# Kernel optimization log

Hardware: AMD Instinct MI355X
Metric: run time of the kernel (lower is better)

## Reference

```python
import jax, jax.numpy as jnp
import numpy as np
from jax import lax

DIM, HEADS, POOL = 512, 8, 16
HD = DIM // HEADS
SCALE = HD ** -0.5


def _cbs(x, w, s, b, d=1, g=1):
    """Conv2d(bias=False, pad=d*(k-1)//2) + folded BN (scale,bias) + SiLU."""
    k = w.shape[-1]
    p = d * (k - 1) // 2
    y = lax.conv_general_dilated(x, w, (1, 1), [(p, p), (p, p)],
                                 rhs_dilation=(d, d), feature_group_count=g,
                                 dimension_numbers=("NCHW", "OIHW", "NCHW"))
    y = y * s[None, :, None, None] + b[None, :, None, None]
    return y * jax.nn.sigmoid(y)  # SiLU


def _forward(x, w01, s01, b01, w02, s02, b02, w03, s03, b03,
             w12, s12, b12, w13, s13, b13, w22, s22, b22, w23, s23, b23,
             w3, s3, b3, wkv, skv, bkv, wfc1, bfc1, wfc2, bfc2):
    bsz, c, h, w = x.shape
    # ---- _MutilScal ----
    a01 = _cbs(x, w01, s01, b01)                       # [b,128,h,w]
    a03 = _cbs(_cbs(a01, w02, s02, b02, d=3, g=128), w03, s03, b03)
    a13 = _cbs(_cbs(a01, w12, s12, b12, d=5, g=128), w13, s13, b13)
    a23 = _cbs(_cbs(a01, w22, s22, b22, d=7, g=128), w23, s23, b23)
    attn = _cbs(a03 + a13 + a23, w3, s3, b3) * x       # [b,512,h,w]
    # AdaptiveAvgPool2d(POOL): exact block mean since h,w divisible by POOL
    pooled = attn.reshape(bsz, c, POOL, h // POOL, POOL, w // POOL).mean(axis=(3, 5))
    kv = _cbs(pooled, wkv, skv, bkv)                   # [b,1024,16,16]
    # ---- pooled cross-attention ----
    n, n1 = h * w, POOL * POOL
    q = x.reshape(bsz, HEADS, HD, n).transpose(0, 1, 3, 2)          # [b,H,n,d]
    kvr = kv.reshape(bsz, 2, HEADS, HD, n1)
    k = kvr[:, 0].transpose(0, 1, 3, 2)                              # [b,H,n1,d]
    v = kvr[:, 1].transpose(0, 1, 3, 2)                              # [b,H,n1,d]
    dots = jnp.einsum("bhnd,bhmd->bhnm", q, k) * SCALE
    a = jax.nn.softmax(dots, axis=-1)
    o = jnp.einsum("bhnm,bhmd->bhnd", a, v)                          # [b,H,n,d]
    attn_out = o.transpose(0, 1, 3, 2).reshape(bsz, c, h, w)
    # ---- SE channel gate ----
    gap = x.mean(axis=(2, 3))                                        # [b,c]
    y = jnp.clip(gap @ wfc1[:, :, 0, 0].T + bfc1, 0.0, 6.0)          # ReLU6
    gate = jax.nn.sigmoid(y @ wfc2[:, :, 0, 0].T + bfc2)             # [b,c]
    c_attn = gate[:, :, None, None] * x
    return attn_out + c_attn


def setup_inputs() -> dict:
    key = jax.random.key(0)
    ks = jax.random.split(key, 32)
    ki = iter(ks)
    f = jnp.float32

    def rn(shape, scale=0.05):
        return (jax.random.normal(next(ki), shape, dtype=f) * scale)

    inp = {"x": jax.random.normal(next(ki), (8, DIM, 64, 64), dtype=f)}
    inp.update(w01=rn((128, 512, 1, 1)), s01=jnp.ones((128,), f), b01=rn((128,)))
    inp.update(w02=rn((128, 1, 3, 3)), s02=jnp.ones((128,), f), b02=rn((128,)))
    inp.update(w03=rn((512, 128, 1, 1)), s03=jnp.ones((512,), f), b03=rn((512,)))
    inp.update(w12=rn((128, 1, 3, 3)), s12=jnp.ones((128,), f), b12=rn((128,)))
    inp.update(w13=rn((512, 128, 1, 1)), s13=jnp.ones((512,), f), b13=rn((512,)))
    inp.update(w22=rn((128, 1, 3, 3)), s22=jnp.ones((128,), f), b22=rn((128,)))
    inp.update(w23=rn((512, 128, 1, 1)), s23=jnp.ones((512,), f), b23=rn((512,)))
    inp.update(w3=rn((512, 512, 1, 1)), s3=jnp.ones((512,), f), b3=rn((512,)))
    inp.update(wkv=rn((1024, 512, 1, 1)), skv=jnp.ones((1024,), f), bkv=rn((1024,)))
    inp.update(wfc1=rn((128, 512, 1, 1)), bfc1=rn((128,)))
    inp.update(wfc2=rn((512, 128, 1, 1)), bfc2=rn((512,)))
    return inp


def reference(x, w01, s01, b01, w02, s02, b02, w03, s03, b03,
              w12, s12, b12, w13, s13, b13, w22, s22, b22, w23, s23, b23,
              w3, s3, b3, wkv, skv, bkv, wfc1, bfc1, wfc2, bfc2):
    return _forward(x, w01, s01, b01, w02, s02, b02, w03, s03, b03,
                    w12, s12, b12, w13, s13, b13, w22, s22, b22, w23, s23, b23,
                    w3, s3, b3, wkv, skv, bkv, wfc1, bfc1, wfc2, bfc2)
```

## Files before the change

kernel.cpp:

```cpp
#include <hip/hip_runtime.h>
#include <cstddef>


static __device__ __forceinline__ float silu_f(float v) {
  return v / (1.f + __expf(-v));
}

typedef __attribute__((ext_vector_type(8))) short short8v;
typedef __attribute__((ext_vector_type(4))) float f32x4;

union FragU { unsigned u[4]; short8v v; uint4 q; };

static __device__ __forceinline__ unsigned short f2bf(float f) {
  unsigned u = __builtin_bit_cast(unsigned, f);
  u += 0x7fffu + ((u >> 16) & 1u);
  return (unsigned short)(u >> 16);
}
static __device__ __forceinline__ unsigned packbf(float lo, float hi) {
  return (unsigned)f2bf(lo) | ((unsigned)f2bf(hi) << 16);
}
static __device__ __forceinline__ float bf_lo(unsigned w) {
  return __builtin_bit_cast(float, w << 16);
}
static __device__ __forceinline__ float bf_hi(unsigned w) {
  return __builtin_bit_cast(float, w & 0xffff0000u);
}

static __device__ __forceinline__ void gload16(const unsigned* gsrc, unsigned* ldst) {
  __builtin_amdgcn_global_load_lds(
      (const __attribute__((address_space(1))) unsigned*)gsrc,
      (__attribute__((address_space(3))) unsigned*)ldst, 16, 0, 0);
}

static __device__ __forceinline__ void stage_tile_g(const unsigned* __restrict__ src,
                                                    unsigned* dst, int tid) {
  gload16(src + 4 * tid, dst + 4 * tid);
  gload16(src + 4 * (tid + 512), dst + 4 * (tid + 512));
}

static __device__ __forceinline__ short8v load_frag4(const unsigned* P, int ksg, int pos) {
  FragU f;
  f.q = *(const uint4*)(P + (((ksg << 7) + pos) << 2));
  return f.v;
}

static __device__ __forceinline__ void stage_x_pack(const float* __restrict__ src, int ld,
                                                    unsigned* Xp, int tid) {
  const int pos = tid & 127, kg = tid >> 7;
  const float* p = src + pos + (size_t)(kg * 16) * ld;
  float v[16];
#pragma unroll
  for (int i = 0; i < 16; ++i) v[i] = p[(size_t)i * ld];
#pragma unroll
  for (int i2 = 0; i2 < 4; ++i2) {
    const int kq = kg * 4 + i2;
    const int r4 = (kq & 3) + ((kq >> 3) << 2);
    const int sub = (kq >> 2) & 1;
    uint2 wv;
    wv.x = packbf(v[i2 * 4 + 0], v[i2 * 4 + 1]);
    wv.y = packbf(v[i2 * 4 + 2], v[i2 * 4 + 3]);
    *(uint2*)(Xp + (((r4 << 7) + pos) << 2) + sub * 2) = wv;
  }
}

#define GEMM_IDS                                            \
  const int tid = threadIdx.x;                              \
  const int w = tid >> 6, lane = tid & 63;                  \
  const int g = lane >> 4, nl = lane & 15;                  \
  const int wr = w >> 1, wc = w & 1;

#define GEMM_KSTEP(ACC)                                                            \
  _Pragma("unroll")                                                                \
  for (int ks = 0; ks < 2; ++ks) {                                                 \
    const short8v a0 = load_frag4(Wp, ks * 4 + g, wr * 32 + nl);                   \
    const short8v a1 = load_frag4(Wp, ks * 4 + g, wr * 32 + 16 + nl);              \
    _Pragma("unroll")                                                              \
    for (int jj = 0; jj < 4; ++jj) {                                               \
      const short8v bfr = load_frag4(Xp, ks * 4 + g, wc * 64 + jj * 16 + nl);      \
      ACC[0][jj] = __builtin_amdgcn_mfma_f32_16x16x32_bf16(a0, bfr, ACC[0][jj], 0, 0, 0); \
      ACC[1][jj] = __builtin_amdgcn_mfma_f32_16x16x32_bf16(a1, bfr, ACC[1][jj], 0, 0, 0); \
    }                                                                              \
  }

__global__ __launch_bounds__(256)
void prepack_w_kernel(const float* __restrict__ w01, const float* __restrict__ w03,
                      const float* __restrict__ w13, const float* __restrict__ w23,
                      const float* __restrict__ w3, const float* __restrict__ wkv,
                      unsigned* __restrict__ img)
{
  const int t = blockIdx.x;
  const float* W; int K; int tile; unsigned* base;
  if (t < 8)       { W = w01; K = 512; tile = t;      base = img; }
  else if (t < 16) { W = w03; K = 128; tile = t - 8;  base = img + 32768; }
  else if (t < 24) { W = w13; K = 128; tile = t - 16; base = img + 65536; }
  else if (t < 32) { W = w23; K = 128; tile = t - 24; base = img + 98304; }
  else if (t < 64) { W = w3;  K = 512; tile = t - 32; base = img + 131072; }
  else             { W = wkv; K = 512; tile = t - 64; base = img + 262144; }
  const int nk = K >> 6;
  const int to = tile / nk, tk = tile - to * nk;
  unsigned* dst = base + (size_t)tile * 4096;
  for (int wi = threadIdx.x; wi < 4096; wi += 256) {
    const int r4 = wi >> 9, pos = (wi >> 2) & 127, sub = (wi >> 1) & 1, j = wi & 1;
    const int kq = (r4 & 3) + sub * 4 + ((r4 >> 2) << 3);
    const int k = tk * 64 + 4 * kq + 2 * j;
    const int oc = to * 128 + pos;
    dst[wi] = packbf(W[(size_t)oc * K + k], W[(size_t)oc * K + k + 1]);
  }
}

__global__ __launch_bounds__(512)
void gemm_a01_kernel(const float* __restrict__ X, const unsigned* __restrict__ Wimg,
                     const float* __restrict__ sc, const float* __restrict__ bi,
                     unsigned* __restrict__ A01p)
{
  const int b = blockIdx.z, p0 = blockIdx.x * 128;
  GEMM_IDS
  __shared__ unsigned Xp[4096], Wp[4096];

  f32x4 acc[2][4];
#pragma unroll
  for (int i = 0; i < 2; ++i)
#pragma unroll
    for (int jj = 0; jj < 4; ++jj) acc[i][jj] = (f32x4){0.f, 0.f, 0.f, 0.f};

  for (int ks8 = 0; ks8 < 8; ++ks8) {
    __syncthreads();
    stage_x_pack(X + (size_t)b * 512 * 4096 + (size_t)(ks8 * 64) * 4096 + p0, 4096, Xp, tid);
    stage_tile_g(Wimg + (size_t)ks8 * 4096, Wp, tid);
    __syncthreads();
    GEMM_KSTEP(acc)
  }

#pragma unroll
  for (int i = 0; i < 2; ++i) {
    const int base = wr * 32 + i * 16 + 4 * g;
    const float s0_ = sc[base + 0], b0_ = bi[base + 0];
    const float s1_ = sc[base + 1], b1_ = bi[base + 1];
    const float s2_ = sc[base + 2], b2_ = bi[base + 2];
    const float s3_ = sc[base + 3], b3_ = bi[base + 3];
#pragma unroll
    for (int jj = 0; jj < 4; ++jj) {
      const int pos = p0 + wc * 64 + jj * 16 + nl;
      const float v0 = silu_f(s0_ * acc[i][jj][0] + b0_);
      const float v1 = silu_f(s1_ * acc[i][jj][1] + b1_);
      const float v2 = silu_f(s2_ * acc[i][jj][2] + b2_);
      const float v3 = silu_f(s3_ * acc[i][jj][3] + b3_);
      A01p[((size_t)b * 64 + (base >> 1)) * 4096 + pos]     = packbf(v0, v1);
      A01p[((size_t)b * 64 + (base >> 1) + 1) * 4096 + pos] = packbf(v2, v3);
    }
  }
}

__global__ __launch_bounds__(256)
void dwconv_pack_kernel(const unsigned* __restrict__ A01p, unsigned* __restrict__ Timg,
                        const float* __restrict__ w02, const float* __restrict__ s02, const float* __restrict__ b02,
                        const float* __restrict__ w12, const float* __restrict__ s12, const float* __restrict__ b12,
                        const float* __restrict__ w22, const float* __restrict__ s22, const float* __restrict__ b22)
{
  const int br = blockIdx.z;
  const int yb = blockIdx.y;
  const int b = yb >> 4, t16 = yb & 15, kstep = t16 >> 3, mm = t16 & 7;
  const int kq = (mm & 3) + ((mm >> 2) << 3);
  const int cbase = kstep * 64 + kq * 4;
  const int p = blockIdx.x * 256 + threadIdx.x;
  const int y = p >> 6, xx = p & 63;
  const int d = 3 + 2 * br;

  const float* wsel = br == 0 ? w02 : (br == 1 ? w12 : w22);
  const float* ssel = br == 0 ? s02 : (br == 1 ? s12 : s22);
  const float* bsel = br == 0 ? b02 : (br == 1 ? b12 : b22);

  float sum[8] = {};
  const unsigned* plane0 = A01p + ((size_t)b * 64 + (cbase >> 1)) * 4096;

#pragma unroll
  for (int u = -1; u <= 1; ++u) {
    const int yv = y + u * d;
    if ((unsigned)yv < 64u) {
#pragma unroll
      for (int v = -1; v <= 1; ++v) {
        const int xv = xx + v * d;
        if ((unsigned)xv < 64u) {
          const int idx = yv * 64 + xv;
          const int tap = (u + 1) * 3 + (v + 1);
#pragma unroll
          for (int q = 0; q < 4; ++q) {
            const int sub = q >> 1, jw = q & 1;
            const unsigned wv = plane0[(size_t)(sub * 8 + jw) * 4096 + idx];
            const int ch = cbase + sub * 16 + jw * 2;
            sum[q * 2 + 0] += wsel[(ch + 0) * 9 + tap] * bf_lo(wv);
            sum[q * 2 + 1] += wsel[(ch + 1) * 9 + tap] * bf_hi(wv);
          }
        }
      }
    }
  }

  unsigned wout[4];
#pragma unroll
  for (int h = 0; h < 4; ++h) {
    const int ch = cbase + (h >> 1) * 16 + (h & 1) * 2;
    const float va = silu_f(ssel[ch] * sum[h * 2] + bsel[ch]);
    const float vb = silu_f(ssel[ch + 1] * sum[h * 2 + 1] + bsel[ch + 1]);
    wout[h] = packbf(va, vb);
  }
  const int tile = ((br * 8 + b) * 2 + kstep) * 32 + (p >> 7);
  *(uint4*)(Timg + (size_t)tile * 4096 + (((mm << 7) + (p & 127)) << 2)) = *(uint4*)wout;
}

__global__ __launch_bounds__(512)
void gemm3branch_img_kernel(const unsigned* __restrict__ Timg, const unsigned* __restrict__ Wimg3,
                            const float* __restrict__ s0, const float* __restrict__ s1, const float* __restrict__ s2,
                            const float* __restrict__ b0, const float* __restrict__ b1, const float* __restrict__ b2,
                            unsigned* __restrict__ Bimg)
{
  const int b = blockIdx.z, pt = blockIdx.x, oc0 = blockIdx.y * 128;
  GEMM_IDS
  __shared__ unsigned Xp[4096], Wp[4096];

  float sum[2][4][4] = {};

#pragma unroll
  for (int brn = 0; brn < 3; ++brn) {
    const float* ss = brn == 0 ? s0 : (brn == 1 ? s1 : s2);
    const float* bs = brn == 0 ? b0 : (brn == 1 ? b1 : b2);

    f32x4 acc[2][4];
#pragma unroll
    for (int i = 0; i < 2; ++i)
#pragma unroll
      for (int jj = 0; jj < 4; ++jj) acc[i][jj] = (f32x4){0.f, 0.f, 0.f, 0.f};

#pragma unroll
    for (int ksx = 0; ksx < 2; ++ksx) {
      __syncthreads();
      stage_tile_g(Timg + (((size_t)(brn * 8 + b) * 2 + ksx) * 32 + pt) * 4096, Xp, tid);
      stage_tile_g(Wimg3 + (size_t)brn * 32768 + ((size_t)(oc0 >> 7) * 2 + ksx) * 4096, Wp, tid);
      __syncthreads();
      GEMM_KSTEP(acc)
    }

#pragma unroll
    for (int i = 0; i < 2; ++i) {
      const int base = oc0 + wr * 32 + i * 16 + 4 * g;
#pragma unroll
      for (int r = 0; r < 4; ++r) {
        const float s = ss[base + r], bb = bs[base + r];
#pragma unroll
        for (int jj = 0; jj < 4; ++jj)
          sum[i][jj][r] += silu_f(s * acc[i][jj][r] + bb);
      }
    }
  }

#pragma unroll
  for (int i = 0; i < 2; ++i) {
    const int ol = wr * 32 + i * 16 + 4 * g;
    const int kstep_g = (oc0 + ol) >> 6;
    const int kin = ol & 63;
    const int kq2 = kin >> 2;
    const int r4 = (kq2 & 3) + ((kq2 >> 3) << 2);
    const int sub = (kq2 >> 2) & 1;
#pragma unroll
    for (int jj = 0; jj < 4; ++jj) {
      const int pos = wc * 64 + jj * 16 + nl;
      uint2 wv;
      wv.x = packbf(sum[i][jj][0], sum[i][jj][1]);
      wv.y = packbf(sum[i][jj][2], sum[i][jj][3]);
      *(uint2*)(Bimg + ((size_t)(b * 8 + kstep_g) * 32 + pt) * 4096 + (((r4 << 7) + pos) << 2) + sub * 2) = wv;
    }
  }
}

__global__ __launch_bounds__(512)
void gemm_pool_img_kernel(const unsigned* __restrict__ Bimg, const unsigned* __restrict__ W3img,
                          const float* __restrict__ sc, const float* __restrict__ bi,
                          const float* __restrict__ xin, float* __restrict__ pooled)
{
  const int b = blockIdx.z, pt = blockIdx.x, oc0 = blockIdx.y * 128;
  const int p0 = pt * 128;
  const float* xb = xin + (size_t)b * 512 * 4096;
  GEMM_IDS
  __shared__ unsigned Xp[4096], Wp[4096];

  f32x4 acc[2][4];
#pragma unroll
  for (int i = 0; i < 2; ++i)
#pragma unroll
    for (int jj = 0; jj < 4; ++jj) acc[i][jj] = (f32x4){0.f, 0.f, 0.f, 0.f};

  for (int ks8 = 0; ks8 < 8; ++ks8) {
    __syncthreads();
    stage_tile_g(Bimg + ((size_t)(b * 8 + ks8) * 32 + pt) * 4096, Xp, tid);
    stage_tile_g(W3img + ((size_t)(oc0 >> 7) * 8 + ks8) * 4096, Wp, tid);
    __syncthreads();
    GEMM_KSTEP(acc)
  }

#pragma unroll
  for (int i = 0; i < 2; ++i)
#pragma unroll
    for (int r = 0; r < 4; ++r) {
      const int oc = oc0 + wr * 32 + i * 16 + 4 * g + r;
      const float s = sc[oc], bb = bi[oc];
#pragma unroll
      for (int jj = 0; jj < 4; ++jj) {
        const int p = p0 + wc * 64 + jj * 16 + nl;
        float val = silu_f(s * acc[i][jj][r] + bb) * xb[(size_t)oc * 4096 + p];
        val += __shfl_xor(val, 1, 64);
        val += __shfl_xor(val, 2, 64);
        if ((nl & 3) == 0) {
          const int y = p >> 6, col = p & 63;
          atomicAdd(&pooled[((size_t)b * 512 + oc) * 256 + (y >> 2) * 16 + (col >> 2)],
                    val * (1.f / 16.f));
        }
      }
    }
}

__global__ __launch_bounds__(512)
void gemm_kv_kernel(const float* __restrict__ X, const unsigned* __restrict__ WKVimg,
                    const float* __restrict__ sc, const float* __restrict__ bi,
                    unsigned* __restrict__ Kimg, unsigned* __restrict__ Vimg)
{
  const int b = blockIdx.z, p0 = blockIdx.x * 128, oc0 = blockIdx.y * 128;
  const float* Xb = X + (size_t)b * 512 * 256;
  GEMM_IDS
  __shared__ unsigned Xp[4096], Wp[4096];

  f32x4 acc[2][4];
#pragma unroll
  for (int i = 0; i < 2; ++i)
#pragma unroll
    for (int jj = 0; jj < 4; ++jj) acc[i][jj] = (f32x4){0.f, 0.f, 0.f, 0.f};

  for (int ks8 = 0; ks8 < 8; ++ks8) {
    __syncthreads();
    stage_x_pack(Xb + (size_t)(ks8 * 64) * 256 + p0, 256, Xp, tid);
    stage_tile_g(WKVimg + ((size_t)(oc0 >> 7) * 8 + ks8) * 4096, Wp, tid);
    __syncthreads();
    GEMM_KSTEP(acc)
  }

  const bool isK = (oc0 < 512);
#pragma unroll
  for (int i = 0; i < 2; ++i) {
    const int ocb = oc0 + wr * 32 + i * 16 + 4 * g;
#pragma unroll
    for (int jj = 0; jj < 4; ++jj) {
      const int pos = p0 + wc * 64 + jj * 16 + nl;
      float v[4];
#pragma unroll
      for (int r = 0; r < 4; ++r)
        v[r] = silu_f(sc[ocb + r] * acc[i][jj][r] + bi[ocb + r]);
      const int ch = pos >> 7, ml = pos & 127;
      if (isK) {
        const int h = ocb >> 6, d0 = ocb & 63;
        const int kq = d0 >> 2, sub = (kq >> 2) & 1;
        const int r4 = (kq & 3) + ((kq >> 3) << 2);
        unsigned* t = Kimg + ((size_t)(b * 8 + h) * 2 + ch) * 4096;
        uint2 wv;
        wv.x = packbf(v[0] * 0.125f, v[1] * 0.125f);
        wv.y = packbf(v[2] * 0.125f, v[3] * 0.125f);
        *(uint2*)(t + (((r4 << 7) + ml) << 2) + sub * 2) = wv;
      } else {
        const int h = (ocb - 512) >> 6, d0 = (ocb - 512) & 63;
        unsigned* t = Vimg + ((size_t)(b * 8 + h) * 2 + ch) * 4096;
        float ov[4];
#pragma unroll
        for (int r = 0; r < 4; ++r) ov[r] = __shfl_xor(v[r], 1, 64);
        if ((nl & 1) == 0) {
          const int s = (ml >> 1) & 1, m4 = ml >> 2;
#pragma unroll
          for (int r = 0; r < 4; ++r)
            t[((m4 * 64 + d0 + r) << 1) + s] = packbf(v[r], ov[r]);
        }
      }
    }
  }
}

__global__ __launch_bounds__(256)
void gap_kernel(const float* __restrict__ x, float* __restrict__ gap)
{
  const int bc = blockIdx.x;
  const int tid = threadIdx.x;
  const float* p = x + (size_t)bc * 4096;
  float v = 0.f;
#pragma unroll
  for (int j = 0; j < 16; ++j) v += p[j * 256 + tid];
#pragma unroll
  for (int off = 32; off >= 1; off >>= 1) v += __shfl_down(v, off, 64);
  __shared__ float red[4];
  if ((tid & 63) == 0) red[tid >> 6] = v;
  __syncthreads();
  if (tid == 0) gap[bc] = (red[0] + red[1] + red[2] + red[3]) * (1.f / 4096.f);
}

__global__ __launch_bounds__(512)
void se_kernel(const float* __restrict__ gap,
               const float* __restrict__ wfc1, const float* __restrict__ bfc1,
               const float* __restrict__ wfc2, const float* __restrict__ bfc2,
               float* __restrict__ gate)
{
  const int b = blockIdx.x, tid = threadIdx.x;
  __shared__ float ylds[128];
  if (tid < 128) {
    float a = 0.f;
    for (int c = 0; c < 512; ++c) a += gap[b * 512 + c] * wfc1[tid * 512 + c];
    a += bfc1[tid];
    ylds[tid] = fminf(fmaxf(a, 0.f), 6.f);
  }
  __syncthreads();
  float g = 0.f;
  for (int j = 0; j < 128; ++j) g += ylds[j] * wfc2[tid * 128 + j];
  g += bfc2[tid];
  gate[b * 512 + tid] = 1.f / (1.f + __expf(-g));
}

__global__ __launch_bounds__(512)
void attn_mfma_kernel(const float* __restrict__ x, const unsigned* __restrict__ Kimg,
                      const unsigned* __restrict__ Vimg,
                      const float* __restrict__ gate, float* __restrict__ out)
{
  const int b = blockIdx.z, h = blockIdx.y;
  const int n0 = blockIdx.x * 128;
  const int tid = threadIdx.x;
  const int w = tid >> 6, lane = tid & 63;
  const int g = lane >> 4, nl = lane & 15;

  __shared__ unsigned lds[20480];
  unsigned* Qp = lds;
  unsigned* Kb0 = lds + 4096;
  unsigned* Kb1 = lds + 8192;
  unsigned* Vb0 = lds + 12288;
  unsigned* Vb1 = lds + 16384;
  float* Osm = (float*)(lds + 4096);

  const size_t tbase = (size_t)(b * 8 + h) * 2 * 4096;

  stage_tile_g(Kimg + tbase, Kb0, tid);
  stage_tile_g(Vimg + tbase, Vb0, tid);
  stage_x_pack(x + ((size_t)b * 512 + h * 64) * 4096 + n0, 4096, Qp, tid);
  __syncthreads();
  stage_tile_g(Kimg + tbase + 4096, Kb1, tid);
  stage_tile_g(Vimg + tbase + 4096, Vb1, tid);

  float m_run = -1e30f, l_run = 0.f;
  f32x4 o[4];
#pragma unroll
  for (int i = 0; i < 4; ++i) o[i] = (f32x4){0.f, 0.f, 0.f, 0.f};

#pragma unroll
  for (int ch = 0; ch < 2; ++ch) {
    const unsigned* Kp = ch ? Kb1 : Kb0;
    const unsigned* Vp = ch ? Vb1 : Vb0;

    f32x4 s[8];
#pragma unroll
    for (int mb = 0; mb < 8; ++mb) s[mb] = (f32x4){0.f, 0.f, 0.f, 0.f};
#pragma unroll
    for (int ks = 0; ks < 2; ++ks) {
      const short8v qf = load_frag4(Qp, ks * 4 + g, w * 16 + nl);
#pragma unroll
      for (int mb = 0; mb < 8; ++mb) {
        const short8v kf = load_frag4(Kp, ks * 4 + g, mb * 16 + nl);
        s[mb] = __builtin_amdgcn_mfma_f32_16x16x32_bf16(kf, qf, s[mb], 0, 0, 0);
      }
    }

    float cm = -1e30f;
#pragma unroll
    for (int mb = 0; mb < 8; ++mb)
#pragma unroll
      for (int r = 0; r < 4; ++r) cm = fmaxf(cm, s[mb][r]);
    cm = fmaxf(cm, __shfl_xor(cm, 16, 64));
    cm = fmaxf(cm, __shfl_xor(cm, 32, 64));
    const float mnew = fmaxf(m_run, cm);
    const float corr = __expf(m_run - mnew);
    m_run = mnew;
    float cs = 0.f;
#pragma unroll
    for (int mb = 0; mb < 8; ++mb)
#pragma unroll
      for (int r = 0; r < 4; ++r) {
        const float p = __expf(s[mb][r] - mnew);
        s[mb][r] = p;
        cs += p;
      }
    cs += __shfl_xor(cs, 16, 64);
    cs += __shfl_xor(cs, 32, 64);
    l_run = l_run * corr + cs;
#pragma unroll
    for (int db = 0; db < 4; ++db)
#pragma unroll
      for (int r = 0; r < 4; ++r) o[db][r] *= corr;

#pragma unroll
    for (int ks = 0; ks < 4; ++ks) {
      FragU pf;
      pf.u[0] = packbf(s[2 * ks][0],     s[2 * ks][1]);
      pf.u[1] = packbf(s[2 * ks][2],     s[2 * ks][3]);
      pf.u[2] = packbf(s[2 * ks + 1][0], s[2 * ks + 1][1]);
      pf.u[3] = packbf(s[2 * ks + 1][2], s[2 * ks + 1][3]);
#pragma unroll
      for (int db = 0; db < 4; ++db) {
        FragU vf;
        const uint2 lo = *(const uint2*)(Vp + ((8 * ks + g) * 64 + db * 16 + nl) * 2);
        const uint2 hi = *(const uint2*)(Vp + ((8 * ks + 4 + g) * 64 + db * 16 + nl) * 2);
        vf.u[0] = lo.x; vf.u[1] = lo.y; vf.u[2] = hi.x; vf.u[3] = hi.y;
        o[db] = __builtin_amdgcn_mfma_f32_16x16x32_bf16(vf.v, pf.v, o[db], 0, 0, 0);
      }
    }
    __syncthreads();
  }

  const float inv = 1.f / l_run;
#pragma unroll
  for (int db = 0; db < 4; ++db)
#pragma unroll
    for (int r = 0; r < 4; ++r)
      Osm[(db * 16 + 4 * g + r) * 132 + w * 16 + nl] = o[db][r] * inv;
  __syncthreads();

  {
    const int n = tid & 127, t7 = tid >> 7;
    const int jw = t7 >> 1, half = t7 & 1;
#pragma unroll
    for (int i = 0; i < 16; ++i) {
      const int d = t7 + 4 * i;
      const int r4 = (i & 3) + ((i >> 3) << 2);
      const int sub = (i >> 2) & 1;
      const unsigned xw = Qp[(((r4 << 7) + n) << 2) + sub * 2 + jw];
      const float xv = half ? bf_hi(xw) : bf_lo(xw);
      const int c2 = h * 64 + d;
      const size_t off = ((size_t)b * 512 + c2) * 4096 + n0 + n;
      out[off] = Osm[d * 132 + n] + gate[b * 512 + c2] * xv;
    }
  }
}

extern "C" void kernel_launch(void* const* d_in, const int* in_sizes, int n_in,
                              void* d_out, int out_size, void* d_ws, size_t ws_size,
                              hipStream_t stream)
{
  const float* x    = (const float*)d_in[0];
  const float* w01  = (const float*)d_in[1];
  const float* s01  = (const float*)d_in[2];
  const float* b01  = (const float*)d_in[3];
  const float* w02  = (const float*)d_in[4];
  const float* s02  = (const float*)d_in[5];
  const float* b02  = (const float*)d_in[6];
  const float* w03  = (const float*)d_in[7];
  const float* s03  = (const float*)d_in[8];
  const float* b03  = (const float*)d_in[9];
  const float* w12  = (const float*)d_in[10];
  const float* s12  = (const float*)d_in[11];
  const float* b12  = (const float*)d_in[12];
  const float* w13  = (const float*)d_in[13];
  const float* s13  = (const float*)d_in[14];
  const float* b13  = (const float*)d_in[15];
  const float* w22  = (const float*)d_in[16];
  const float* s22  = (const float*)d_in[17];
  const float* b22  = (const float*)d_in[18];
  const float* w23  = (const float*)d_in[19];
  const float* s23  = (const float*)d_in[20];
  const float* b23  = (const float*)d_in[21];
  const float* w3   = (const float*)d_in[22];
  const float* s3   = (const float*)d_in[23];
  const float* b3   = (const float*)d_in[24];
  const float* wkv  = (const float*)d_in[25];
  const float* skv  = (const float*)d_in[26];
  const float* bkv  = (const float*)d_in[27];
  const float* wfc1 = (const float*)d_in[28];
  const float* bfc1 = (const float*)d_in[29];
  const float* wfc2 = (const float*)d_in[30];
  const float* bfc2 = (const float*)d_in[31];

  float* out = (float*)d_out;
  unsigned* wsu = (unsigned*)d_ws;

  unsigned* Timg   = wsu;
  float*    pooled = (float*)(wsu + 6291456);
  unsigned* Kimg   = wsu + 7340032;
  unsigned* Vimg   = wsu + 7864320;
  float*    gapb   = (float*)(wsu + 8388608);
  float*    gateb  = (float*)(wsu + 8392704);
  unsigned* Wimg   = wsu + 8396800;

  unsigned* A01p = (unsigned*)d_out;
  unsigned* Bimg = (unsigned*)d_out;

  prepack_w_kernel<<<128, 256, 0, stream>>>(w01, w03, w13, w23, w3, wkv, Wimg);
  gemm_a01_kernel<<<dim3(32, 1, 8), 512, 0, stream>>>(x, Wimg, s01, b01, A01p);
  dwconv_pack_kernel<<<dim3(16, 128, 3), 256, 0, stream>>>(A01p, Timg,
      w02, s02, b02, w12, s12, b12, w22, s22, b22);
  gemm3branch_img_kernel<<<dim3(32, 4, 8), 512, 0, stream>>>(Timg, Wimg + 32768,
      s03, s13, s23, b03, b13, b23, Bimg);
  hipMemsetAsync(pooled, 0, (size_t)1048576 * sizeof(float), stream);
  gemm_pool_img_kernel<<<dim3(32, 4, 8), 512, 0, stream>>>(Bimg, Wimg + 131072,
      s3, b3, x, pooled);
  gemm_kv_kernel<<<dim3(2, 8, 8), 512, 0, stream>>>(pooled, Wimg + 262144, skv, bkv, Kimg, Vimg);
  gap_kernel<<<4096, 256, 0, stream>>>(x, gapb);
  se_kernel<<<8, 512, 0, stream>>>(gapb, wfc1, bfc1, wfc2, bfc2, gateb);
  attn_mfma_kernel<<<dim3(32, 8, 8), 512, 0, stream>>>(x, Kimg, Vimg, gateb, out);
}
```

Baseline: 280.0 us.

## Double-buffer LDS tiles in GEMM kernels to overlap loads with MFMA

Four GEMM kernels now use two LDS buffers for the X and W tiles. Each loop step issues the next tile's global loads (async global_load_lds, plus register prefetch of the fp32 X values) before running the MFMAs on the current buffer, and keeps one barrier per step instead of two. The three-branch kernel is flattened into a single six-step pipelined loop, with the per-branch SiLU epilogue folded in. The aim is to hide global-memory latency behind compute, at the cost of twice the shared memory per block, which may lower occupancy, and more registers for the prefetched X values.

```diff
diff --git a/kernel.cpp b/kernel.cpp
--- a/kernel.cpp
+++ b/kernel.cpp
@@ -44,13 +44,15 @@
   return f.v;
 }
 
-static __device__ __forceinline__ void stage_x_pack(const float* __restrict__ src, int ld,
-                                                    unsigned* Xp, int tid) {
+static __device__ __forceinline__ void xload16(const float* __restrict__ src, int ld,
+                                               int tid, float v[16]) {
   const int pos = tid & 127, kg = tid >> 7;
   const float* p = src + pos + (size_t)(kg * 16) * ld;
-  float v[16];
 #pragma unroll
   for (int i = 0; i < 16; ++i) v[i] = p[(size_t)i * ld];
+}
+static __device__ __forceinline__ void xwrite16(const float v[16], unsigned* Xp, int tid) {
+  const int pos = tid & 127, kg = tid >> 7;
 #pragma unroll
   for (int i2 = 0; i2 < 4; ++i2) {
     const int kq = kg * 4 + i2;
@@ -63,20 +65,27 @@
   }
 }
 
+static __device__ __forceinline__ void stage_x_pack(const float* __restrict__ src, int ld,
+                                                    unsigned* Xp, int tid) {
+  float v[16];
+  xload16(src, ld, tid, v);
+  xwrite16(v, Xp, tid);
+}
+
 #define GEMM_IDS                                            \
   const int tid = threadIdx.x;                              \
   const int w = tid >> 6, lane = tid & 63;                  \
   const int g = lane >> 4, nl = lane & 15;                  \
   const int wr = w >> 1, wc = w & 1;
 
-#define GEMM_KSTEP(ACC)                                                            \
+#define GEMM_KSTEP_B(ACC, XB, WB)                                                  \
   _Pragma("unroll")                                                                \
   for (int ks = 0; ks < 2; ++ks) {                                                 \
-    const short8v a0 = load_frag4(Wp, ks * 4 + g, wr * 32 + nl);                   \
-    const short8v a1 = load_frag4(Wp, ks * 4 + g, wr * 32 + 16 + nl);              \
+    const short8v a0 = load_frag4(WB, ks * 4 + g, wr * 32 + nl);                   \
+    const short8v a1 = load_frag4(WB, ks * 4 + g, wr * 32 + 16 + nl);              \
     _Pragma("unroll")                                                              \
     for (int jj = 0; jj < 4; ++jj) {                                               \
-      const short8v bfr = load_frag4(Xp, ks * 4 + g, wc * 64 + jj * 16 + nl);      \
+      const short8v bfr = load_frag4(XB, ks * 4 + g, wc * 64 + jj * 16 + nl);      \
       ACC[0][jj] = __builtin_amdgcn_mfma_f32_16x16x32_bf16(a0, bfr, ACC[0][jj], 0, 0, 0); \
       ACC[1][jj] = __builtin_amdgcn_mfma_f32_16x16x32_bf16(a1, bfr, ACC[1][jj], 0, 0, 0); \
     }                                                                              \
@@ -115,7 +124,8 @@
 {
   const int b = blockIdx.z, p0 = blockIdx.x * 128;
   GEMM_IDS
-  __shared__ unsigned Xp[4096], Wp[4096];
+  __shared__ unsigned Xp[2][4096], Wp[2][4096];
+  const float* Xbase = X + (size_t)b * 512 * 4096 + p0;
 
   f32x4 acc[2][4];
 #pragma unroll
@@ -123,12 +133,24 @@
 #pragma unroll
     for (int jj = 0; jj < 4; ++jj) acc[i][jj] = (f32x4){0.f, 0.f, 0.f, 0.f};
 
-  for (int ks8 = 0; ks8 < 8; ++ks8) {
+  {
+    float vx[16];
+    xload16(Xbase, 4096, tid, vx);
+    stage_tile_g(Wimg, Wp[0], tid);
+    xwrite16(vx, Xp[0], tid);
+  }
+  __syncthreads();
+
+  for (int st = 0; st < 8; ++st) {
+    const int cur = st & 1;
+    float vn[16];
+    if (st < 7) {
+      xload16(Xbase + (size_t)((st + 1) * 64) * 4096, 4096, tid, vn);
+      stage_tile_g(Wimg + (size_t)(st + 1) * 4096, Wp[cur ^ 1], tid);
+    }
+    GEMM_KSTEP_B(acc, Xp[cur], Wp[cur])
+    if (st < 7) xwrite16(vn, Xp[cur ^ 1], tid);
     __syncthreads();
-    stage_x_pack(X + (size_t)b * 512 * 4096 + (size_t)(ks8 * 64) * 4096 + p0, 4096, Xp, tid);
-    stage_tile_g(Wimg + (size_t)ks8 * 4096, Wp, tid);
-    __syncthreads();
-    GEMM_KSTEP(acc)
   }
 
 #pragma unroll
@@ -216,42 +238,51 @@
 {
   const int b = blockIdx.z, pt = blockIdx.x, oc0 = blockIdx.y * 128;
   GEMM_IDS
-  __shared__ unsigned Xp[4096], Wp[4096];
+  __shared__ unsigned Xp[2][4096], Wp[2][4096];
 
   float sum[2][4][4] = {};
-
-#pragma unroll
-  for (int brn = 0; brn < 3; ++brn) {
-    const float* ss = brn == 0 ? s0 : (brn == 1 ? s1 : s2);
-    const float* bs = brn == 0 ? b0 : (brn == 1 ? b1 : b2);
-
-    f32x4 acc[2][4];
-#pragma unroll
-    for (int i = 0; i < 2; ++i)
-#pragma unroll
-      for (int jj = 0; jj < 4; ++jj) acc[i][jj] = (f32x4){0.f, 0.f, 0.f, 0.f};
-
-#pragma unroll
-    for (int ksx = 0; ksx < 2; ++ksx) {
-      __syncthreads();
-      stage_tile_g(Timg + (((size_t)(brn * 8 + b) * 2 + ksx) * 32 + pt) * 4096, Xp, tid);
-      stage_tile_g(Wimg3 + (size_t)brn * 32768 + ((size_t)(oc0 >> 7) * 2 + ksx) * 4096, Wp, tid);
-      __syncthreads();
-      GEMM_KSTEP(acc)
-    }
-
-#pragma unroll
-    for (int i = 0; i < 2; ++i) {
-      const int base = oc0 + wr * 32 + i * 16 + 4 * g;
-#pragma unroll
-      for (int r = 0; r < 4; ++r) {
-        const float s = ss[base + r], bb = bs[base + r];
-#pragma unroll
-        for (int jj = 0; jj < 4; ++jj)
-          sum[i][jj][r] += silu_f(s * acc[i][jj][r] + bb);
+  f32x4 acc[2][4];
+#pragma unroll
+  for (int i = 0; i < 2; ++i)
+#pragma unroll
+    for (int jj = 0; jj < 4; ++jj) acc[i][jj] = (f32x4){0.f, 0.f, 0.f, 0.f};
+
+#define SRC_X3(st) (Timg + (((size_t)(((st) >> 1) * 8 + b) * 2 + ((st) & 1)) * 32 + pt) * 4096)
+#define SRC_W3(st) (Wimg3 + (size_t)((st) >> 1) * 32768 + ((size_t)(oc0 >> 7) * 2 + ((st) & 1)) * 4096)
+
+  stage_tile_g(SRC_X3(0), Xp[0], tid);
+  stage_tile_g(SRC_W3(0), Wp[0], tid);
+  __syncthreads();
+
+  for (int st = 0; st < 6; ++st) {
+    const int cur = st & 1;
+    if (st < 5) {
+      stage_tile_g(SRC_X3(st + 1), Xp[cur ^ 1], tid);
+      stage_tile_g(SRC_W3(st + 1), Wp[cur ^ 1], tid);
+    }
+    GEMM_KSTEP_B(acc, Xp[cur], Wp[cur])
+    if (st & 1) {
+      const int brn = st >> 1;
+      const float* ss = brn == 0 ? s0 : (brn == 1 ? s1 : s2);
+      const float* bs = brn == 0 ? b0 : (brn == 1 ? b1 : b2);
+#pragma unroll
+      for (int i = 0; i < 2; ++i) {
+        const int base = oc0 + wr * 32 + i * 16 + 4 * g;
+#pragma unroll
+        for (int r = 0; r < 4; ++r) {
+          const float s = ss[base + r], bb = bs[base + r];
+#pragma unroll
+          for (int jj = 0; jj < 4; ++jj) {
+            sum[i][jj][r] += silu_f(s * acc[i][jj][r] + bb);
+            acc[i][jj][r] = 0.f;
+          }
+        }
       }
     }
-  }
+    __syncthreads();
+  }
+#undef SRC_X3
+#undef SRC_W3
 
 #pragma unroll
   for (int i = 0; i < 2; ++i) {
@@ -281,7 +312,7 @@
   const int p0 = pt * 128;
   const float* xb = xin + (size_t)b * 512 * 4096;
   GEMM_IDS
-  __shared__ unsigned Xp[4096], Wp[4096];
+  __shared__ unsigned Xp[2][4096], Wp[2][4096];
 
   f32x4 acc[2][4];
 #pragma unroll
@@ -289,13 +320,24 @@
 #pragma unroll
     for (int jj = 0; jj < 4; ++jj) acc[i][jj] = (f32x4){0.f, 0.f, 0.f, 0.f};
 
-  for (int ks8 = 0; ks8 < 8; ++ks8) {
+#define SRC_XP(st) (Bimg + ((size_t)(b * 8 + (st)) * 32 + pt) * 4096)
+#define SRC_WP(st) (W3img + ((size_t)(oc0 >> 7) * 8 + (st)) * 4096)
+
+  stage_tile_g(SRC_XP(0), Xp[0], tid);
+  stage_tile_g(SRC_WP(0), Wp[0], tid);
+  __syncthreads();
+
+  for (int st = 0; st < 8; ++st) {
+    const int cur = st & 1;
+    if (st < 7) {
+      stage_tile_g(SRC_XP(st + 1), Xp[cur ^ 1], tid);
+      stage_tile_g(SRC_WP(st + 1), Wp[cur ^ 1], tid);
+    }
+    GEMM_KSTEP_B(acc, Xp[cur], Wp[cur])
     __syncthreads();
-    stage_tile_g(Bimg + ((size_t)(b * 8 + ks8) * 32 + pt) * 4096, Xp, tid);
-    stage_tile_g(W3img + ((size_t)(oc0 >> 7) * 8 + ks8) * 4096, Wp, tid);
-    __syncthreads();
-    GEMM_KSTEP(acc)
-  }
+  }
+#undef SRC_XP
+#undef SRC_WP
 
 #pragma unroll
   for (int i = 0; i < 2; ++i)
@@ -324,9 +366,9 @@
                     unsigned* __restrict__ Kimg, unsigned* __restrict__ Vimg)
 {
   const int b = blockIdx.z, p0 = blockIdx.x * 128, oc0 = blockIdx.y * 128;
-  const float* Xb = X + (size_t)b * 512 * 256;
+  const float* Xb = X + (size_t)b * 512 * 256 + p0;
   GEMM_IDS
-  __shared__ unsigned Xp[4096], Wp[4096];
+  __shared__ unsigned Xp[2][4096], Wp[2][4096];
 
   f32x4 acc[2][4];
 #pragma unroll
@@ -334,12 +376,24 @@
 #pragma unroll
     for (int jj = 0; jj < 4; ++jj) acc[i][jj] = (f32x4){0.f, 0.f, 0.f, 0.f};
 
-  for (int ks8 = 0; ks8 < 8; ++ks8) {
+  {
+    float vx[16];
+    xload16(Xb, 256, tid, vx);
+    stage_tile_g(WKVimg + (size_t)(oc0 >> 7) * 8 * 4096, Wp[0], tid);
+    xwrite16(vx, Xp[0], tid);
+  }
+  __syncthreads();
+
+  for (int st = 0; st < 8; ++st) {
+    const int cur = st & 1;
+    float vn[16];
+    if (st < 7) {
+      xload16(Xb + (size_t)((st + 1) * 64) * 256, 256, tid, vn);
+      stage_tile_g(WKVimg + ((size_t)(oc0 >> 7) * 8 + st + 1) * 4096, Wp[cur ^ 1], tid);
+    }
+    GEMM_KSTEP_B(acc, Xp[cur], Wp[cur])
+    if (st < 7) xwrite16(vn, Xp[cur ^ 1], tid);
     __syncthreads();
-    stage_x_pack(Xb + (size_t)(ks8 * 64) * 256 + p0, 256, Xp, tid);
-    stage_tile_g(WKVimg + ((size_t)(oc0 >> 7) * 8 + ks8) * 4096, Wp, tid);
-    __syncthreads();
-    GEMM_KSTEP(acc)
   }
 
   const bool isK = (oc0 < 512);
```

Measured after the change: 256.3 us. 8.5% less time.
